# Performance work log

Hardware: AMD Instinct MI355X
Metric: run time of the kernel (lower is better)

Reference implementation:

```python
import jax, jax.numpy as jnp
import numpy as np

EPS = 1e-6
ALPHA = 0.2  # LeakyReLU negative slope


def layer_norm(x, g, b):
    mu = jnp.mean(x, axis=-1, keepdims=True)
    var = jnp.mean(jnp.square(x - mu), axis=-1, keepdims=True)
    return (x - mu) * jax.lax.rsqrt(var + EPS) * g + b


def graph_attention(x, bias, W, a_src, a_dst):
    # x: [B,N,D], bias: [B,N,N], W: [D, H*Dh], a_src/a_dst: [H, Dh]
    B, N, D = x.shape
    H, Dh = a_src.shape
    h = jnp.einsum('bnd,dhk->bhnk', x, W.reshape(D, H, Dh))  # [B,H,N,Dh]
    s = jnp.einsum('bhnk,hk->bhn', h, a_src)                 # source term
    t = jnp.einsum('bhnk,hk->bhn', h, a_dst)                 # target term
    e = jax.nn.leaky_relu(s[:, :, :, None] + t[:, :, None, :], ALPHA)
    e = e + bias[:, None, :, :]                              # graph mask/bias
    attn = jax.nn.softmax(e, axis=-1)                        # [B,H,N,N]
    out = jnp.einsum('bhij,bhjk->bhik', attn, h)             # [B,H,N,Dh]
    return out.transpose(0, 2, 1, 3).reshape(B, N, H * Dh)


def setup_inputs() -> dict:
    key = jax.random.key(0)
    ks = jax.random.split(key, 8)
    B, N, D, H = 2, 2048, 512, 8
    Dh = D // H
    sc = 1.0 / np.sqrt(D)
    return {
        'x': jax.random.normal(ks[0], (B, N, D), jnp.float32),
        'bias': jax.random.normal(ks[1], (B, N, N), jnp.float32),
        'W1': jax.random.normal(ks[2], (D, D), jnp.float32) * sc,
        'a_src1': jax.random.normal(ks[3], (H, Dh), jnp.float32) * sc,
        'a_dst1': jax.random.normal(ks[4], (H, Dh), jnp.float32) * sc,
        'g1': jnp.ones((D,), jnp.float32),
        'b1': jnp.zeros((D,), jnp.float32),
        'W2': jax.random.normal(ks[5], (D, D), jnp.float32) * sc,
        'a_src2': jax.random.normal(ks[6], (1, D), jnp.float32) * sc,
        'a_dst2': jax.random.normal(ks[7], (1, D), jnp.float32) * sc,
        'g2': jnp.ones((D,), jnp.float32),
        'b2': jnp.zeros((D,), jnp.float32),
    }


def reference(x, bias, W1, a_src1, a_dst1, g1, b1, W2, a_src2, a_dst2, g2, b2):
    # dropout is identity in eval mode
    attn_in = layer_norm(x, g1, b1)
    attn = graph_attention(attn_in, bias, W1, a_src1, a_dst1) + x
    attn_in2 = layer_norm(attn, g2, b2)
    out = graph_attention(attn_in2, bias, W2, a_src2, a_dst2) + attn
    return out
```

## Files before the change

### kernel.cpp

```cpp
#include <hip/hip_runtime.h>
#include <math.h>

#define NB 2
#define NN 2048
#define DD 512
#define L2E 1.44269504088896340736f

typedef __attribute__((ext_vector_type(8))) short short8;
typedef __attribute__((ext_vector_type(4))) float f32x4;

__device__ __forceinline__ unsigned short f2bf(float x) {
  union { float f; unsigned u; } a;
  a.f = x;
  unsigned r = a.u + 0x7FFF + ((a.u >> 16) & 1);
  return (unsigned short)(r >> 16);
}
__device__ __forceinline__ float bf2f(unsigned short u) {
  union { unsigned u; float f; } a;
  a.u = ((unsigned)u) << 16;
  return a.f;
}
__device__ __forceinline__ unsigned cvtpk(float lo, float hi) {
  unsigned r;
  asm("v_cvt_pk_bf16_f32 %0, %1, %2" : "=v"(r) : "v"(lo), "v"(hi));
  return r;
}
__device__ __forceinline__ uint2 exp4pk(float e0, float e1, float e2, float e3) {
  float p0, p1, p2, p3;
  uint2 d;
  asm("v_exp_f32 %2, %6\n\t"
      "v_exp_f32 %3, %7\n\t"
      "v_exp_f32 %4, %8\n\t"
      "v_exp_f32 %5, %9\n\t"
      "v_cvt_pk_bf16_f32 %0, %2, %3\n\t"
      "v_cvt_pk_bf16_f32 %1, %4, %5"
      : "=&v"(d.x), "=&v"(d.y), "=&v"(p0), "=&v"(p1), "=&v"(p2), "=&v"(p3)
      : "v"(e0), "v"(e1), "v"(e2), "v"(e3));
  return d;
}

__device__ __forceinline__ float waveReduceSum(float v) {
#pragma unroll
  for (int o = 32; o; o >>= 1) v += __shfl_down(v, o, 64);
  return v;
}
__device__ __forceinline__ float blockReduceSum(float v, float* red4) {
  int tid = threadIdx.x;
  __syncthreads();
  v = waveReduceSum(v);
  if ((tid & 63) == 0) red4[tid >> 6] = v;
  __syncthreads();
  return red4[0] + red4[1] + red4[2] + red4[3];
}

__global__ __launch_bounds__(256) void prep_kernel(
    const float* __restrict__ W1, const float* __restrict__ W2,
    unsigned short* __restrict__ WT1, unsigned short* __restrict__ WT2,
    const float* __restrict__ as1, const float* __restrict__ ad1,
    float* __restrict__ vs1, float* __restrict__ vd1,
    const float* __restrict__ as2, const float* __restrict__ ad2,
    float* __restrict__ vs2, float* __restrict__ vd2) {
  __shared__ float tile[64][65];
  int bid = blockIdx.x;
  int t = threadIdx.x;
  if (bid < 128) {
    const float* W = (bid & 64) ? W2 : W1;
    unsigned short* WT = (bid & 64) ? WT2 : WT1;
    int r = bid & 63;
    int kt = (r >> 3) * 64, ct = (r & 7) * 64;
#pragma unroll
    for (int u = 0; u < 16; u++) {
      int lin = t + u * 256;
      int kl = lin >> 6, cl = lin & 63;
      tile[kl][cl] = W[(size_t)(kt + kl) * DD + ct + cl];
    }
    __syncthreads();
#pragma unroll
    for (int u = 0; u < 16; u++) {
      int lin = t + u * 256;
      int cl = lin >> 6, kl = lin & 63;
      WT[(size_t)(ct + cl) * DD + kt + kl] = f2bf(tile[kl][cl]);
    }
  } else {
    int idx = bid - 128;
    int slot = idx >> 3, dch = idx & 7;
    const float *W, *as, *ad;
    float *vs, *vd;
    int Dh, hoff;
    if (slot < 8) {
      W = W1; as = as1 + slot * 64; ad = ad1 + slot * 64;
      vs = vs1 + (size_t)slot * DD; vd = vd1 + (size_t)slot * DD;
      Dh = 64; hoff = slot * 64;
    } else {
      W = W2; as = as2; ad = ad2; vs = vs2; vd = vd2;
      Dh = 512; hoff = 0;
    }
    int dl = t >> 2, kq = t & 3;
    int d = dch * 64 + dl;
    int kn = Dh >> 2;
    const float* wr = W + (size_t)d * DD + hoff + kq * kn;
    const float* asp = as + kq * kn;
    const float* adp = ad + kq * kn;
    float s = 0.f, dd2 = 0.f;
    for (int k = 0; k < kn; k++) {
      float wv = wr[k];
      s += wv * asp[k];
      dd2 += wv * adp[k];
    }
    s += __shfl_xor(s, 1);
    s += __shfl_xor(s, 2);
    dd2 += __shfl_xor(dd2, 1);
    dd2 += __shfl_xor(dd2, 2);
    if (kq == 0) {
      vs[d] = s;
      vd[d] = dd2;
    }
  }
}

__global__ __launch_bounds__(256) void lnst_kernel(
    const float* __restrict__ x, const float* __restrict__ g,
    const float* __restrict__ bb, unsigned short* __restrict__ y,
    const float* __restrict__ vs, const float* __restrict__ vd,
    float* __restrict__ sOut, float* __restrict__ tOut, int HN) {
  __shared__ float red4[4];
  __shared__ float lnS[512];
  int row = blockIdx.x;
  int t = threadIdx.x;
  const float* xr = x + (size_t)row * DD;
  float2 v = *(const float2*)&xr[2 * t];
  float s = blockReduceSum(v.x + v.y, red4);
  float mu = s * (1.0f / 512.0f);
  float d0 = v.x - mu, d1 = v.y - mu;
  float ss = blockReduceSum(d0 * d0 + d1 * d1, red4);
  float rstd = rsqrtf(ss * (1.0f / 512.0f) + 1e-6f);
  float2 gg = *(const float2*)&g[2 * t];
  float2 bv = *(const float2*)&bb[2 * t];
  float n0 = d0 * rstd * gg.x + bv.x;
  float n1 = d1 * rstd * gg.y + bv.y;
  ushort2 o;
  o.x = f2bf(n0);
  o.y = f2bf(n1);
  *(ushort2*)&y[(size_t)row * DD + 2 * t] = o;
  lnS[2 * t] = n0;
  lnS[2 * t + 1] = n1;
  __syncthreads();
  int wv = t >> 6, l = t & 63;
  int b = row >> 11, n = row & (NN - 1);
  float4 x0 = *(const float4*)&lnS[l * 8];
  float4 x1 = *(const float4*)&lnS[l * 8 + 4];
  for (int h = wv; h < HN; h += 4) {
    const float* vsr = vs + (size_t)h * DD + l * 8;
    const float* vdr = vd + (size_t)h * DD + l * 8;
    float4 a0 = *(const float4*)vsr, a1 = *(const float4*)(vsr + 4);
    float4 c0 = *(const float4*)vdr, c1 = *(const float4*)(vdr + 4);
    float ps = x0.x * a0.x + x0.y * a0.y + x0.z * a0.z + x0.w * a0.w +
               x1.x * a1.x + x1.y * a1.y + x1.z * a1.z + x1.w * a1.w;
    float pd = x0.x * c0.x + x0.y * c0.y + x0.z * c0.z + x0.w * c0.w +
               x1.x * c1.x + x1.y * c1.y + x1.z * c1.z + x1.w * c1.w;
#pragma unroll
    for (int o2 = 32; o2; o2 >>= 1) {
      ps += __shfl_xor(ps, o2);
      pd += __shfl_xor(pd, o2);
    }
    if (l == 0) {
      sOut[((size_t)b * HN + h) * NN + n] = ps * L2E;
      tOut[((size_t)b * HN + h) * NN + n] = pd * L2E;
    }
  }
}

__global__ __launch_bounds__(256) void gemm_kernel(const unsigned short* __restrict__ A,
                                                   const unsigned short* __restrict__ BT,
                                                   unsigned short* __restrict__ hbT) {
  __shared__ float accL[4][16][65];
  int t = threadIdx.x, w = t >> 6, l = t & 63;
  int li = l & 15, lg = l >> 4;
  int R0 = blockIdx.x * 16;
  int c0 = blockIdx.y * 64;
  const unsigned short* ar = A + (size_t)(R0 + li) * DD + w * 128 + lg * 8;
  const unsigned short* br = BT + (size_t)(c0 + li) * DD + w * 128 + lg * 8;
  f32x4 acc[4] = {};
#pragma unroll
  for (int k0 = 0; k0 < 128; k0 += 32) {
    short8 af = *(const short8*)(ar + k0);
#pragma unroll
    for (int f = 0; f < 4; f++) {
      short8 bf = *(const short8*)(br + (size_t)f * 16 * DD + k0);
      acc[f] = __builtin_amdgcn_mfma_f32_16x16x32_bf16(af, bf, acc[f], 0, 0, 0);
    }
  }
#pragma unroll
  for (int f = 0; f < 4; f++)
#pragma unroll
    for (int r = 0; r < 4; r++) accL[w][lg * 4 + r][f * 16 + li] = acc[f][r];
  __syncthreads();
  int b = R0 >> 11, jT = (R0 & (NN - 1)) >> 4;
#pragma unroll
  for (int u = 0; u < 2; u++) {
    int idx = t + u * 256;
    int f = idx >> 7;
    int rem = idx & 127;
    int cl = rem >> 3, jlp = rem & 7;
    int cc = f * 16 + cl;
    float v0 = accL[0][2 * jlp][cc] + accL[1][2 * jlp][cc] + accL[2][2 * jlp][cc] +
               accL[3][2 * jlp][cc];
    float v1 = accL[0][2 * jlp + 1][cc] + accL[1][2 * jlp + 1][cc] +
               accL[2][2 * jlp + 1][cc] + accL[3][2 * jlp + 1][cc];
    size_t off = (((size_t)(b * (DD / 64) + blockIdx.y) * (NN / 16)) + jT) * 1024 +
                 f * 256 + cl * 16 + jlp * 2;
    *(unsigned*)(hbT + off) = cvtpk(v0, v1);
  }
}

template <int HN, int CCH>
__global__ __launch_bounds__(256) void pv_kernel(
    const unsigned short* __restrict__ hbT, const float* __restrict__ bias,
    const float* __restrict__ sArr, const float* __restrict__ tArr,
    const float* __restrict__ res, float* __restrict__ out) {
  constexpr int DH = DD / HN;
  __shared__ unsigned short Pl[4][2][1024];
  __shared__ float accL[4][16][33];
  __shared__ float sLa[4][16];
  int t = threadIdx.x, w = t >> 6, l = t & 63;
  int li = l & 15, lg = l >> 4;
  int i0 = blockIdx.x * 16;
  int ck = blockIdx.y, bh = blockIdx.z;
  int h = bh % HN, b = bh / HN;
  int c0 = h * DH + ck * (CCH * 64);
  size_t bhN = (size_t)bh * NN;
  const float* trow = tArr + bhN;

  int rs = l >> 3;
  int js = (l & 7) * 8;
  int jc = l & 7;
  int wchunk = ((jc & 4) | ((jc & 3) ^ (rs & 3))) * 8;
  float sv[2];
  sv[0] = sArr[bhN + i0 + rs];
  sv[1] = sArr[bhN + i0 + 8 + rs];
  const float* bb0 = bias + ((size_t)b * NN + i0 + rs) * NN;
  const float* bb1 = bb0 + (size_t)8 * NN;

  const unsigned short* vbase =
      hbT + ((size_t)(b * (DD / 64) + (c0 >> 6)) * (NN / 16)) * 1024 +
      (lg >> 1) * 1024 + li * 16 + (lg & 1) * 8;
  int ra0 = li * 64 + ((lg ^ (li & 3))) * 8;
  int ra1 = ra0 + 32;

  union { short8 v; unsigned short q[8]; } ones;
#pragma unroll
  for (int k = 0; k < 8; k++) ones.q[k] = 0x3F80;

  const int jbeg = w * (NN / 4), jend = jbeg + NN / 4;
  f32x4 acc[CCH][4] = {};
  f32x4 accS = {0.f, 0.f, 0.f, 0.f};

  auto loadTB = [&](int j, float4& t0, float4& t1, float4& b0a, float4& b0b,
                    float4& b1a, float4& b1b) {
    t0 = *(const float4*)&trow[j + js];
    t1 = *(const float4*)&trow[j + js + 4];
    b0a = *(const float4*)&bb0[j + js];
    b0b = *(const float4*)&bb0[j + js + 4];
    b1a = *(const float4*)&bb1[j + js];
    b1b = *(const float4*)&bb1[j + js + 4];
  };
  auto computeP = [&](const float4& t0, const float4& t1, const float4& b0a,
                      const float4& b0b, const float4& b1a, const float4& b1b, int pb) {
#pragma unroll
    for (int u = 0; u < 2; u++) {
      const float4& ba = u ? b1a : b0a;
      const float4& bc = u ? b1b : b0b;
      int row = u * 8 + rs;
      float e0 = sv[u] + t0.x, e1 = sv[u] + t0.y;
      float e2 = sv[u] + t0.z, e3 = sv[u] + t0.w;
      float e4 = sv[u] + t1.x, e5 = sv[u] + t1.y;
      float e6 = sv[u] + t1.z, e7 = sv[u] + t1.w;
      e0 = fmaf(ba.x, L2E, fmaxf(e0, 0.2f * e0));
      e1 = fmaf(ba.y, L2E, fmaxf(e1, 0.2f * e1));
      e2 = fmaf(ba.z, L2E, fmaxf(e2, 0.2f * e2));
      e3 = fmaf(ba.w, L2E, fmaxf(e3, 0.2f * e3));
      e4 = fmaf(bc.x, L2E, fmaxf(e4, 0.2f * e4));
      e5 = fmaf(bc.y, L2E, fmaxf(e5, 0.2f * e5));
      e6 = fmaf(bc.z, L2E, fmaxf(e6, 0.2f * e6));
      e7 = fmaf(bc.w, L2E, fmaxf(e7, 0.2f * e7));
      uint2 d0 = exp4pk(e0, e1, e2, e3);
      uint2 d1 = exp4pk(e4, e5, e6, e7);
      uint4 dd;
      dd.x = d0.x; dd.y = d0.y; dd.z = d1.x; dd.w = d1.y;
      *(uint4*)&Pl[w][pb][row * 64 + wchunk] = dd;
    }
  };
  auto loadV = [&](int jt, short8 (&vv)[CCH][8]) {
#pragma unroll
    for (int cc = 0; cc < CCH; cc++) {
      const unsigned short* vp =
          vbase + (size_t)cc * ((NN / 16) * 1024) + (size_t)jt * 64;
#pragma unroll
      for (int f = 0; f < 4; f++) {
        vv[cc][f] = *(const short8*)(vp + f * 256);
        vv[cc][4 + f] = *(const short8*)(vp + 2048 + f * 256);
      }
    }
  };
  auto domfma = [&](short8 a0, short8 a1, const short8 (&vv)[CCH][8]) {
    __builtin_amdgcn_s_setprio(1);
    accS = __builtin_amdgcn_mfma_f32_16x16x32_bf16(a0, ones.v, accS, 0, 0, 0);
#pragma unroll
    for (int cc = 0; cc < CCH; cc++)
#pragma unroll
      for (int f = 0; f < 4; f++)
        acc[cc][f] =
            __builtin_amdgcn_mfma_f32_16x16x32_bf16(a0, vv[cc][f], acc[cc][f], 0, 0, 0);
    accS = __builtin_amdgcn_mfma_f32_16x16x32_bf16(a1, ones.v, accS, 0, 0, 0);
#pragma unroll
    for (int cc = 0; cc < CCH; cc++)
#pragma unroll
      for (int f = 0; f < 4; f++)
        acc[cc][f] =
            __builtin_amdgcn_mfma_f32_16x16x32_bf16(a1, vv[cc][4 + f], acc[cc][f], 0, 0, 0);
    __builtin_amdgcn_s_setprio(0);
  };

  float4 tA0, tA1, bA0, bA1, bA2, bA3;
  short8 vv[CCH][8];

  loadTB(jbeg, tA0, tA1, bA0, bA1, bA2, bA3);
  computeP(tA0, tA1, bA0, bA1, bA2, bA3, 0);
  loadTB(jbeg + 64, tA0, tA1, bA0, bA1, bA2, bA3);

  int buf = 0;
  for (int jt = jbeg; jt < jend; jt += 64) {
    loadV(jt, vv);
    short8 a0 = *(const short8*)&Pl[w][buf][ra0];
    short8 a1 = *(const short8*)&Pl[w][buf][ra1];
    if (jt + 64 < jend) {
      float4 n0 = tA0, n1 = tA1, m0 = bA0, m1 = bA1, m2 = bA2, m3 = bA3;
      int jn = (jt + 128 < jend) ? (jt + 128) : jbeg;
      loadTB(jn, tA0, tA1, bA0, bA1, bA2, bA3);
      computeP(n0, n1, m0, m1, m2, m3, buf ^ 1);
    }
    domfma(a0, a1, vv);
    buf ^= 1;
  }

  if (li == 0) {
#pragma unroll
    for (int r = 0; r < 4; r++) sLa[w][lg * 4 + r] = accS[r];
  }
#pragma unroll
  for (int g = 0; g < 2 * CCH; g++) {
    int cc = g >> 1, half = g & 1;
#pragma unroll
    for (int f = 0; f < 2; f++)
#pragma unroll
      for (int r = 0; r < 4; r++)
        accL[w][lg * 4 + r][f * 16 + li] = acc[cc][half * 2 + f][r];
    __syncthreads();
    {
      int rr = t >> 4, cp = (t & 15) * 2;
      float S = sLa[0][rr] + sLa[1][rr] + sLa[2][rr] + sLa[3][rr];
      float inv = 1.0f / S;
      float2 O = {0.f, 0.f};
#pragma unroll
      for (int w2 = 0; w2 < 4; w2++) {
        O.x += accL[w2][rr][cp];
        O.y += accL[w2][rr][cp + 1];
      }
      size_t ix = ((size_t)b * NN + i0 + rr) * DD + c0 + cc * 64 + half * 32 + cp;
      float2 rv = *(const float2*)&res[ix];
      float2 ov = {O.x * inv + rv.x, O.y * inv + rv.y};
      *(float2*)&out[ix] = ov;
    }
    __syncthreads();
  }
}

extern "C" void kernel_launch(void* const* d_in, const int* in_sizes, int n_in,
                              void* d_out, int out_size, void* d_ws, size_t ws_size,
                              hipStream_t stream) {
  const float* x = (const float*)d_in[0];
  const float* bias = (const float*)d_in[1];
  const float* W1 = (const float*)d_in[2];
  const float* asrc1 = (const float*)d_in[3];
  const float* adst1 = (const float*)d_in[4];
  const float* g1 = (const float*)d_in[5];
  const float* b1 = (const float*)d_in[6];
  const float* W2 = (const float*)d_in[7];
  const float* asrc2 = (const float*)d_in[8];
  const float* adst2 = (const float*)d_in[9];
  const float* g2 = (const float*)d_in[10];
  const float* b2 = (const float*)d_in[11];
  float* out = (float*)d_out;
  float* ws = (float*)d_ws;

  const size_t RC = (size_t)NB * NN * DD;
  float* attnBuf = ws;
  unsigned short* lnB = (unsigned short*)(ws + RC);
  unsigned short* hbT = (unsigned short*)(ws + RC + RC / 2);
  unsigned short* WT1 = (unsigned short*)(ws + 2 * RC);
  unsigned short* WT2 = WT1 + (size_t)DD * DD;
  float* vs1 = (float*)(WT2 + (size_t)DD * DD);
  float* vd1 = vs1 + 8 * DD;
  float* vs2 = vd1 + 8 * DD;
  float* vd2 = vs2 + DD;
  float* sBuf = vd2 + DD;
  float* tBuf = sBuf + 16 * NN;

  const int rows = NB * NN;

  hipLaunchKernelGGL(prep_kernel, dim3(128 + 72), dim3(256), 0, stream, W1, W2, WT1, WT2,
                     asrc1, adst1, vs1, vd1, asrc2, adst2, vs2, vd2);

  hipLaunchKernelGGL(lnst_kernel, dim3(rows), dim3(256), 0, stream, x, g1, b1, lnB, vs1, vd1,
                     sBuf, tBuf, 8);
  hipLaunchKernelGGL(gemm_kernel, dim3(256, 8), dim3(256), 0, stream, lnB, WT1, hbT);
  hipLaunchKernelGGL((pv_kernel<8, 1>), dim3(128, 1, 16), dim3(256), 0, stream, hbT, bias,
                     sBuf, tBuf, x, attnBuf);

  hipLaunchKernelGGL(lnst_kernel, dim3(rows), dim3(256), 0, stream, attnBuf, g2, b2, lnB, vs2,
                     vd2, sBuf, tBuf, 1);
  hipLaunchKernelGGL(gemm_kernel, dim3(256, 8), dim3(256), 0, stream, lnB, WT2, hbT);
  hipLaunchKernelGGL((pv_kernel<1, 2>), dim3(128, 4, 2), dim3(256), 0, stream, hbT, bias,
                     sBuf, tBuf, attnBuf, out);
}
```

Before: 153.3 us.

## Add per-head 8-wave PV kernel sharing bias loads and widen layer-2 chunking

Adds a new 512-thread kernel for the multi-head first layer in which each of 8 waves handles one head over the full key range for the same 16 query rows. This lets the bias tile be read once per block through cache across heads, and removes the cross-wave LDS reduction. The second-layer kernel now processes 4 column chunks per block (grid halved in y), so each computed probability tile is reused over more columns. V loads move inline next to the MFMAs. This trades higher register pressure and fewer blocks (256 for layer one) against less redundant exp/bias work.

```diff
diff --git a/kernel.cpp b/kernel.cpp
--- a/kernel.cpp
+++ b/kernel.cpp
@@ -213,27 +213,19 @@
   }
 }
 
-template <int HN, int CCH>
-__global__ __launch_bounds__(256) void pv_kernel(
+__global__ __launch_bounds__(512) void pvh_kernel(
     const unsigned short* __restrict__ hbT, const float* __restrict__ bias,
     const float* __restrict__ sArr, const float* __restrict__ tArr,
     const float* __restrict__ res, float* __restrict__ out) {
-  constexpr int DH = DD / HN;
-  __shared__ unsigned short Pl[4][2][1024];
-  __shared__ float accL[4][16][33];
-  __shared__ float sLa[4][16];
+  __shared__ unsigned short Pl[8][2][1024];
   int t = threadIdx.x, w = t >> 6, l = t & 63;
   int li = l & 15, lg = l >> 4;
-  int i0 = blockIdx.x * 16;
-  int ck = blockIdx.y, bh = blockIdx.z;
-  int h = bh % HN, b = bh / HN;
-  int c0 = h * DH + ck * (CCH * 64);
-  size_t bhN = (size_t)bh * NN;
+  int i0g = blockIdx.x * 16;
+  int b = i0g >> 11, i0 = i0g & (NN - 1);
+  size_t bhN = (size_t)(b * 8 + w) * NN;
   const float* trow = tArr + bhN;
 
-  int rs = l >> 3;
-  int js = (l & 7) * 8;
-  int jc = l & 7;
+  int rs = l >> 3, js = (l & 7) * 8, jc = l & 7;
   int wchunk = ((jc & 4) | ((jc & 3) ^ (rs & 3))) * 8;
   float sv[2];
   sv[0] = sArr[bhN + i0 + rs];
@@ -242,17 +234,16 @@
   const float* bb1 = bb0 + (size_t)8 * NN;
 
   const unsigned short* vbase =
-      hbT + ((size_t)(b * (DD / 64) + (c0 >> 6)) * (NN / 16)) * 1024 +
-      (lg >> 1) * 1024 + li * 16 + (lg & 1) * 8;
-  int ra0 = li * 64 + ((lg ^ (li & 3))) * 8;
+      hbT + ((size_t)(b * 8 + w) * (NN / 16)) * 1024 + (lg >> 1) * 1024 + li * 16 +
+      (lg & 1) * 8;
+  int ra0 = li * 64 + (lg ^ (li & 3)) * 8;
   int ra1 = ra0 + 32;
 
   union { short8 v; unsigned short q[8]; } ones;
 #pragma unroll
   for (int k = 0; k < 8; k++) ones.q[k] = 0x3F80;
 
-  const int jbeg = w * (NN / 4), jend = jbeg + NN / 4;
-  f32x4 acc[CCH][4] = {};
+  f32x4 acc[4] = {};
   f32x4 accS = {0.f, 0.f, 0.f, 0.f};
 
   auto loadTB = [&](int j, float4& t0, float4& t1, float4& b0a, float4& b0b,
@@ -290,39 +281,133 @@
       *(uint4*)&Pl[w][pb][row * 64 + wchunk] = dd;
     }
   };
-  auto loadV = [&](int jt, short8 (&vv)[CCH][8]) {
-#pragma unroll
-    for (int cc = 0; cc < CCH; cc++) {
-      const unsigned short* vp =
-          vbase + (size_t)cc * ((NN / 16) * 1024) + (size_t)jt * 64;
-#pragma unroll
-      for (int f = 0; f < 4; f++) {
-        vv[cc][f] = *(const short8*)(vp + f * 256);
-        vv[cc][4 + f] = *(const short8*)(vp + 2048 + f * 256);
-      }
-    }
-  };
-  auto domfma = [&](short8 a0, short8 a1, const short8 (&vv)[CCH][8]) {
+
+  float4 tA0, tA1, bA0, bA1, bA2, bA3;
+
+  loadTB(0, tA0, tA1, bA0, bA1, bA2, bA3);
+  computeP(tA0, tA1, bA0, bA1, bA2, bA3, 0);
+  loadTB(64, tA0, tA1, bA0, bA1, bA2, bA3);
+
+  int buf = 0;
+  for (int jt = 0; jt < NN; jt += 64) {
+    const unsigned short* vp = vbase + (size_t)jt * 64;
+    short8 v0 = *(const short8*)(vp + 0);
+    short8 v1 = *(const short8*)(vp + 256);
+    short8 v2 = *(const short8*)(vp + 512);
+    short8 v3 = *(const short8*)(vp + 768);
+    short8 v4 = *(const short8*)(vp + 2048);
+    short8 v5 = *(const short8*)(vp + 2304);
+    short8 v6 = *(const short8*)(vp + 2560);
+    short8 v7 = *(const short8*)(vp + 2816);
+    short8 a0 = *(const short8*)&Pl[w][buf][ra0];
+    short8 a1 = *(const short8*)&Pl[w][buf][ra1];
+    if (jt + 64 < NN) {
+      float4 n0 = tA0, n1 = tA1, m0 = bA0, m1 = bA1, m2 = bA2, m3 = bA3;
+      int jn = (jt + 128 < NN) ? (jt + 128) : 0;
+      loadTB(jn, tA0, tA1, bA0, bA1, bA2, bA3);
+      computeP(n0, n1, m0, m1, m2, m3, buf ^ 1);
+    }
     __builtin_amdgcn_s_setprio(1);
     accS = __builtin_amdgcn_mfma_f32_16x16x32_bf16(a0, ones.v, accS, 0, 0, 0);
-#pragma unroll
-    for (int cc = 0; cc < CCH; cc++)
-#pragma unroll
-      for (int f = 0; f < 4; f++)
-        acc[cc][f] =
-            __builtin_amdgcn_mfma_f32_16x16x32_bf16(a0, vv[cc][f], acc[cc][f], 0, 0, 0);
+    acc[0] = __builtin_amdgcn_mfma_f32_16x16x32_bf16(a0, v0, acc[0], 0, 0, 0);
+    acc[1] = __builtin_amdgcn_mfma_f32_16x16x32_bf16(a0, v1, acc[1], 0, 0, 0);
+    acc[2] = __builtin_amdgcn_mfma_f32_16x16x32_bf16(a0, v2, acc[2], 0, 0, 0);
+    acc[3] = __builtin_amdgcn_mfma_f32_16x16x32_bf16(a0, v3, acc[3], 0, 0, 0);
     accS = __builtin_amdgcn_mfma_f32_16x16x32_bf16(a1, ones.v, accS, 0, 0, 0);
-#pragma unroll
-    for (int cc = 0; cc < CCH; cc++)
-#pragma unroll
-      for (int f = 0; f < 4; f++)
-        acc[cc][f] =
-            __builtin_amdgcn_mfma_f32_16x16x32_bf16(a1, vv[cc][4 + f], acc[cc][f], 0, 0, 0);
+    acc[0] = __builtin_amdgcn_mfma_f32_16x16x32_bf16(a1, v4, acc[0], 0, 0, 0);
+    acc[1] = __builtin_amdgcn_mfma_f32_16x16x32_bf16(a1, v5, acc[1], 0, 0, 0);
+    acc[2] = __builtin_amdgcn_mfma_f32_16x16x32_bf16(a1, v6, acc[2], 0, 0, 0);
+    acc[3] = __builtin_amdgcn_mfma_f32_16x16x32_bf16(a1, v7, acc[3], 0, 0, 0);
     __builtin_amdgcn_s_setprio(0);
+    buf ^= 1;
+  }
+
+#pragma unroll
+  for (int r = 0; r < 4; r++) {
+    float inv = 1.0f / accS[r];
+    size_t ix = ((size_t)b * NN + i0 + lg * 4 + r) * DD + w * 64 + li;
+#pragma unroll
+    for (int f = 0; f < 4; f++) out[ix + f * 16] = acc[f][r] * inv + res[ix + f * 16];
+  }
+}
+
+template <int HN, int CCH>
+__global__ __launch_bounds__(256) void pv_kernel(
+    const unsigned short* __restrict__ hbT, const float* __restrict__ bias,
+    const float* __restrict__ sArr, const float* __restrict__ tArr,
+    const float* __restrict__ res, float* __restrict__ out) {
+  constexpr int DH = DD / HN;
+  __shared__ unsigned short Pl[4][2][1024];
+  __shared__ float accL[4][16][33];
+  __shared__ float sLa[4][16];
+  int t = threadIdx.x, w = t >> 6, l = t & 63;
+  int li = l & 15, lg = l >> 4;
+  int i0 = blockIdx.x * 16;
+  int ck = blockIdx.y, bh = blockIdx.z;
+  int h = bh % HN, b = bh / HN;
+  int c0 = h * DH + ck * (CCH * 64);
+  size_t bhN = (size_t)bh * NN;
+  const float* trow = tArr + bhN;
+
+  int rs = l >> 3, js = (l & 7) * 8, jc = l & 7;
+  int wchunk = ((jc & 4) | ((jc & 3) ^ (rs & 3))) * 8;
+  float sv[2];
+  sv[0] = sArr[bhN + i0 + rs];
+  sv[1] = sArr[bhN + i0 + 8 + rs];
+  const float* bb0 = bias + ((size_t)b * NN + i0 + rs) * NN;
+  const float* bb1 = bb0 + (size_t)8 * NN;
+
+  const unsigned short* vbase =
+      hbT + ((size_t)(b * (DD / 64) + (c0 >> 6)) * (NN / 16)) * 1024 +
+      (lg >> 1) * 1024 + li * 16 + (lg & 1) * 8;
+  int ra0 = li * 64 + (lg ^ (li & 3)) * 8;
+  int ra1 = ra0 + 32;
+
+  union { short8 v; unsigned short q[8]; } ones;
+#pragma unroll
+  for (int k = 0; k < 8; k++) ones.q[k] = 0x3F80;
+
+  const int jbeg = w * (NN / 4), jend = jbeg + NN / 4;
+  f32x4 acc[CCH][4] = {};
+  f32x4 accS = {0.f, 0.f, 0.f, 0.f};
+
+  auto loadTB = [&](int j, float4& t0, float4& t1, float4& b0a, float4& b0b,
+                    float4& b1a, float4& b1b) {
+    t0 = *(const float4*)&trow[j + js];
+    t1 = *(const float4*)&trow[j + js + 4];
+    b0a = *(const float4*)&bb0[j + js];
+    b0b = *(const float4*)&bb0[j + js + 4];
+    b1a = *(const float4*)&bb1[j + js];
+    b1b = *(const float4*)&bb1[j + js + 4];
   };
+  auto computeP = [&](const float4& t0, const float4& t1, const float4& b0a,
+                      const float4& b0b, const float4& b1a, const float4& b1b, int pb) {
+#pragma unroll
+    for (int u = 0; u < 2; u++) {
+      const float4& ba = u ? b1a : b0a;
+      const float4& bc = u ? b1b : b0b;
+      int row = u * 8 + rs;
+      float e0 = sv[u] + t0.x, e1 = sv[u] + t0.y;
+      float e2 = sv[u] + t0.z, e3 = sv[u] + t0.w;
+      float e4 = sv[u] + t1.x, e5 = sv[u] + t1.y;
+      float e6 = sv[u] + t1.z, e7 = sv[u] + t1.w;
+      e0 = fmaf(ba.x, L2E, fmaxf(e0, 0.2f * e0));
+      e1 = fmaf(ba.y, L2E, fmaxf(e1, 0.2f * e1));
+      e2 = fmaf(ba.z, L2E, fmaxf(e2, 0.2f * e2));
+      e3 = fmaf(ba.w, L2E, fmaxf(e3, 0.2f * e3));
+      e4 = fmaf(bc.x, L2E, fmaxf(e4, 0.2f * e4));
+      e5 = fmaf(bc.y, L2E, fmaxf(e5, 0.2f * e5));
+      e6 = fmaf(bc.z, L2E, fmaxf(e6, 0.2f * e6));
+      e7 = fmaf(bc.w, L2E, fmaxf(e7, 0.2f * e7));
+      uint2 d0 = exp4pk(e0, e1, e2, e3);
+      uint2 d1 = exp4pk(e4, e5, e6, e7);
+      uint4 dd;
+      dd.x = d0.x; dd.y = d0.y; dd.z = d1.x; dd.w = d1.y;
+      *(uint4*)&Pl[w][pb][row * 64 + wchunk] = dd;
+    }
+  };
 
   float4 tA0, tA1, bA0, bA1, bA2, bA3;
-  short8 vv[CCH][8];
 
   loadTB(jbeg, tA0, tA1, bA0, bA1, bA2, bA3);
   computeP(tA0, tA1, bA0, bA1, bA2, bA3, 0);
@@ -330,7 +415,6 @@
 
   int buf = 0;
   for (int jt = jbeg; jt < jend; jt += 64) {
-    loadV(jt, vv);
     short8 a0 = *(const short8*)&Pl[w][buf][ra0];
     short8 a1 = *(const short8*)&Pl[w][buf][ra1];
     if (jt + 64 < jend) {
@@ -339,7 +423,31 @@
       loadTB(jn, tA0, tA1, bA0, bA1, bA2, bA3);
       computeP(n0, n1, m0, m1, m2, m3, buf ^ 1);
     }
-    domfma(a0, a1, vv);
+    __builtin_amdgcn_s_setprio(1);
+    accS = __builtin_amdgcn_mfma_f32_16x16x32_bf16(a0, ones.v, accS, 0, 0, 0);
+    accS = __builtin_amdgcn_mfma_f32_16x16x32_bf16(a1, ones.v, accS, 0, 0, 0);
+#pragma unroll
+    for (int cc = 0; cc < CCH; cc++) {
+      const unsigned short* vp =
+          vbase + (size_t)cc * ((NN / 16) * 1024) + (size_t)jt * 64;
+      short8 v0 = *(const short8*)(vp + 0);
+      short8 v1 = *(const short8*)(vp + 256);
+      short8 v2 = *(const short8*)(vp + 512);
+      short8 v3 = *(const short8*)(vp + 768);
+      acc[cc][0] = __builtin_amdgcn_mfma_f32_16x16x32_bf16(a0, v0, acc[cc][0], 0, 0, 0);
+      acc[cc][1] = __builtin_amdgcn_mfma_f32_16x16x32_bf16(a0, v1, acc[cc][1], 0, 0, 0);
+      acc[cc][2] = __builtin_amdgcn_mfma_f32_16x16x32_bf16(a0, v2, acc[cc][2], 0, 0, 0);
+      acc[cc][3] = __builtin_amdgcn_mfma_f32_16x16x32_bf16(a0, v3, acc[cc][3], 0, 0, 0);
+      short8 v4 = *(const short8*)(vp + 2048);
+      short8 v5 = *(const short8*)(vp + 2304);
+      short8 v6 = *(const short8*)(vp + 2560);
+      short8 v7 = *(const short8*)(vp + 2816);
+      acc[cc][0] = __builtin_amdgcn_mfma_f32_16x16x32_bf16(a1, v4, acc[cc][0], 0, 0, 0);
+      acc[cc][1] = __builtin_amdgcn_mfma_f32_16x16x32_bf16(a1, v5, acc[cc][1], 0, 0, 0);
+      acc[cc][2] = __builtin_amdgcn_mfma_f32_16x16x32_bf16(a1, v6, acc[cc][2], 0, 0, 0);
+      acc[cc][3] = __builtin_amdgcn_mfma_f32_16x16x32_bf16(a1, v7, acc[cc][3], 0, 0, 0);
+    }
+    __builtin_amdgcn_s_setprio(0);
     buf ^= 1;
   }
 
@@ -414,12 +522,12 @@
   hipLaunchKernelGGL(lnst_kernel, dim3(rows), dim3(256), 0, stream, x, g1, b1, lnB, vs1, vd1,
                      sBuf, tBuf, 8);
   hipLaunchKernelGGL(gemm_kernel, dim3(256, 8), dim3(256), 0, stream, lnB, WT1, hbT);
-  hipLaunchKernelGGL((pv_kernel<8, 1>), dim3(128, 1, 16), dim3(256), 0, stream, hbT, bias,
-                     sBuf, tBuf, x, attnBuf);
+  hipLaunchKernelGGL(pvh_kernel, dim3(256), dim3(512), 0, stream, hbT, bias, sBuf, tBuf, x,
+                     attnBuf);
 
   hipLaunchKernelGGL(lnst_kernel, dim3(rows), dim3(256), 0, stream, attnBuf, g2, b2, lnB, vs2,
                      vd2, sBuf, tBuf, 1);
   hipLaunchKernelGGL(gemm_kernel, dim3(256, 8), dim3(256), 0, stream, lnB, WT2, hbT);
-  hipLaunchKernelGGL((pv_kernel<1, 2>), dim3(128, 4, 2), dim3(256), 0, stream, hbT, bias,
+  hipLaunchKernelGGL((pv_kernel<1, 4>), dim3(128, 2, 2), dim3(256), 0, stream, hbT, bias,
                      sBuf, tBuf, attnBuf, out);
 }
```

Result: slower. 160.3 us (+4.5%).
